# Performance work log

Hardware: AMD Instinct MI355X
Metric: run time of the kernel (lower is better)

## Reference

```python
import jax, jax.numpy as jnp
import numpy as np

HEADS = 16
DIM = 1024


def setup_inputs() -> dict:
    key = jax.random.key(0)
    ks = jax.random.split(key, 9)
    B, N, D = 2, 2048, DIM
    s = 1.0 / np.sqrt(D)
    x = jax.random.normal(ks[0], (B, N, D), dtype=jnp.float32)
    Wq = jax.random.normal(ks[1], (D, D), dtype=jnp.float32) * s
    Wk = jax.random.normal(ks[2], (D, D), dtype=jnp.float32) * s
    Wv = jax.random.normal(ks[3], (D, D), dtype=jnp.float32) * s
    Wo = jax.random.normal(ks[4], (D, D), dtype=jnp.float32) * s
    bq = jax.random.normal(ks[5], (D,), dtype=jnp.float32) * 0.01
    bk = jax.random.normal(ks[6], (D,), dtype=jnp.float32) * 0.01
    bv = jax.random.normal(ks[7], (D,), dtype=jnp.float32) * 0.01
    bo = jax.random.normal(ks[8], (D,), dtype=jnp.float32) * 0.01
    return {"x": x, "Wq": Wq, "bq": bq, "Wk": Wk, "bk": bk,
            "Wv": Wv, "bv": bv, "Wo": Wo, "bo": bo}


def reference(x, Wq, bq, Wk, bk, Wv, bv, Wo, bo):
    B, N, D = x.shape
    H = HEADS
    hd = D // H
    scale = hd ** (-0.5)
    # projections; split heads -> [B, H, N, hd]
    q = (x @ Wq + bq).reshape(B, N, H, hd).transpose(0, 2, 1, 3)
    k = (x @ Wk + bk).reshape(B, N, H, hd).transpose(0, 2, 1, 3)
    v = (x @ Wv + bv).reshape(B, N, H, hd).transpose(0, 2, 1, 3)
    # full [B, H, N, N] scores (faithful to naive torch implementation)
    attn = jnp.einsum('bhqd,bhkd->bhqk', q, k) * scale
    attn = jax.nn.softmax(attn, axis=-1)
    # dropout is identity in eval mode
    out = jnp.einsum('bhqk,bhkd->bhqd', attn, v)
    out = out.transpose(0, 2, 1, 3).reshape(B, N, D)
    return out @ Wo + bo
```

## Files before the change

### kernel.cpp

```cpp
#include <hip/hip_runtime.h>

#define HEADS 16
#define HD 64
#define SEQ 2048
#define DMODEL 1024
#define BATCH 2
#define MTOT (BATCH*SEQ)
#define KVB 64
#define NKH 16

typedef unsigned short u16;
typedef __bf16 bf16;
typedef bf16 bf16x8 __attribute__((ext_vector_type(8)));
typedef float f32x4 __attribute__((ext_vector_type(4)));
typedef float f32x16 __attribute__((ext_vector_type(16)));
typedef unsigned short u16x8 __attribute__((ext_vector_type(8)));
typedef unsigned short u16x4 __attribute__((ext_vector_type(4)));

static __device__ __forceinline__ u16 f2bf(float f) {
  bf16 b = (bf16)f;
  return __builtin_bit_cast(u16, b);
}

static __device__ __forceinline__ void async16(u16* lds_base, const u16* g) {
  __builtin_amdgcn_global_load_lds(
      (const __attribute__((address_space(1))) unsigned int*)g,
      (__attribute__((address_space(3))) unsigned int*)lds_base,
      16, 0, 0);
}

__global__ __launch_bounds__(256) void k_cvt(const float* __restrict__ in,
                                             u16* __restrict__ out, int n8) {
  int i = blockIdx.x * blockDim.x + threadIdx.x;
  if (i >= n8) return;
  const float4* p = (const float4*)(in + (size_t)i * 8);
  float4 a = p[0], b = p[1];
  u16x8 r;
  r[0] = f2bf(a.x); r[1] = f2bf(a.y); r[2] = f2bf(a.z); r[3] = f2bf(a.w);
  r[4] = f2bf(b.x); r[5] = f2bf(b.y); r[6] = f2bf(b.z); r[7] = f2bf(b.w);
  *(u16x8*)(out + (size_t)i * 8) = r;
}

__global__ __launch_bounds__(256) void k_cvtT(const float* __restrict__ W0, const float* __restrict__ W1,
                                              const float* __restrict__ W2, const float* __restrict__ W3,
                                              u16* __restrict__ T0, u16* __restrict__ T1,
                                              u16* __restrict__ T2, u16* __restrict__ T3) {
  const float* W = blockIdx.z == 0 ? W0 : blockIdx.z == 1 ? W1 : blockIdx.z == 2 ? W2 : W3;
  u16*         T = blockIdx.z == 0 ? T0 : blockIdx.z == 1 ? T1 : blockIdx.z == 2 ? T2 : T3;
  __shared__ u16 tile[64 * 68];
  int t = threadIdx.x;
  int kb = blockIdx.y * 64, nb = blockIdx.x * 64;
#pragma unroll
  for (int i = 0; i < 4; ++i) {
    int c = t * 4 + i;
    int row = c >> 4;
    int c4 = c & 15;
    float4 v = *(const float4*)&W[(size_t)(kb + row) * DMODEL + nb + c4 * 4];
    tile[row * 68 + c4 * 4 + 0] = f2bf(v.x);
    tile[row * 68 + c4 * 4 + 1] = f2bf(v.y);
    tile[row * 68 + c4 * 4 + 2] = f2bf(v.z);
    tile[row * 68 + c4 * 4 + 3] = f2bf(v.w);
  }
  __syncthreads();
#pragma unroll
  for (int i = 0; i < 2; ++i) {
    int c = t * 2 + i;
    int n = c >> 3;
    int k8 = c & 7;
    u16x8 v;
#pragma unroll
    for (int e = 0; e < 8; ++e) v[e] = tile[(k8 * 8 + e) * 68 + n];
    *(u16x8*)&T[(size_t)(nb + n) * DMODEL + kb + k8 * 8] = v;
  }
}

template <int MODE>
__global__ __launch_bounds__(256) void k_gemm(
    const u16* __restrict__ A,
    const u16* __restrict__ BT0, const u16* __restrict__ BT1, const u16* __restrict__ BT2,
    const float* __restrict__ b0, const float* __restrict__ b1, const float* __restrict__ b2,
    void* __restrict__ O0, void* __restrict__ O1, void* __restrict__ O2,
    int M, int N, int K) {
  const u16* BT = blockIdx.z == 0 ? BT0 : blockIdx.z == 1 ? BT1 : BT2;
  const float* bias = blockIdx.z == 0 ? b0 : blockIdx.z == 1 ? b1 : b2;
  void* Out = blockIdx.z == 0 ? O0 : blockIdx.z == 1 ? O1 : O2;

  __shared__ u16 Ads[2][128 * 32];
  __shared__ u16 Bds[2][128 * 32];
  int tid = threadIdx.x, wid = tid >> 6, lane = tid & 63;
  int r = lane & 15, g = lane >> 4;
  int wm = wid >> 1, wn = wid & 1;
  int m0 = blockIdx.y * 128, n0 = blockIdx.x * 128;

  f32x4 acc[4][4];
  f32x4 zero4 = {0.f, 0.f, 0.f, 0.f};
#pragma unroll
  for (int mt = 0; mt < 4; ++mt)
#pragma unroll
    for (int nt = 0; nt < 4; ++nt) acc[mt][nt] = zero4;

  int srow = lane >> 2;
  int scb = lane & 3;

  auto STAGE = [&](int b, int k0) {
#pragma unroll
    for (int tt = 0; tt < 2; ++tt) {
      int inst = wid * 2 + tt;
      int row = inst * 16 + srow;
      async16(&Ads[b][inst * 512], &A[(size_t)(m0 + row) * K + k0 + scb * 8]);
      async16(&Bds[b][inst * 512], &BT[(size_t)(n0 + row) * K + k0 + scb * 8]);
    }
  };

  auto BODY = [&](int buf, int k0) {
    if (k0 + 32 < K) STAGE(buf ^ 1, k0 + 32);
    bf16x8 af[4], bfv[4];
#pragma unroll
    for (int mt = 0; mt < 4; ++mt)
      af[mt] = *(const bf16x8*)&Ads[buf][(wm * 64 + mt * 16 + r) * 32 + g * 8];
#pragma unroll
    for (int nt = 0; nt < 4; ++nt)
      bfv[nt] = *(const bf16x8*)&Bds[buf][(wn * 64 + nt * 16 + r) * 32 + g * 8];
#pragma unroll
    for (int mt = 0; mt < 4; ++mt)
#pragma unroll
      for (int nt = 0; nt < 4; ++nt)
        acc[mt][nt] = __builtin_amdgcn_mfma_f32_16x16x32_bf16(af[mt], bfv[nt], acc[mt][nt], 0, 0, 0);
    asm volatile("s_waitcnt vmcnt(0)" ::: "memory");
    __builtin_amdgcn_sched_barrier(0);
    __builtin_amdgcn_s_barrier();
    __builtin_amdgcn_sched_barrier(0);
  };

  STAGE(0, 0);
  asm volatile("s_waitcnt vmcnt(0)" ::: "memory");
  __builtin_amdgcn_sched_barrier(0);
  __builtin_amdgcn_s_barrier();
  __builtin_amdgcn_sched_barrier(0);

  for (int k0 = 0; k0 < K; k0 += 64) {
    BODY(0, k0);
    BODY(1, k0 + 32);
  }

  const float qs = 0.18033688011112042f;
#pragma unroll
  for (int nt = 0; nt < 4; ++nt) {
    int col = n0 + wn * 64 + nt * 16 + r;
    float bv = bias[col];
#pragma unroll
    for (int mt = 0; mt < 4; ++mt) {
      int rowb = m0 + wm * 64 + mt * 16 + g * 4;
      if (MODE == 0) {
        int b = rowb >> 11;
        int h = col >> 6, d = col & (HD - 1);
        if (blockIdx.z == 2) {
          int n = rowb & (SEQ - 1);
          int np = (n & ~12) | ((n & 4) << 1) | ((n & 8) >> 1);
          u16x4 pk;
#pragma unroll
          for (int j = 0; j < 4; ++j) pk[j] = f2bf(acc[mt][nt][j] + bv);
          *(u16x4*)&((u16*)Out)[((size_t)((b * HEADS + h) * HD + d)) * SEQ + np] = pk;
        } else {
          float sc = (blockIdx.z == 0) ? qs : 1.0f;
#pragma unroll
          for (int j = 0; j < 4; ++j) {
            int row = rowb + j;
            int n = row & (SEQ - 1);
            ((u16*)Out)[((size_t)(b * HEADS + h) * SEQ + n) * HD + d] = f2bf((acc[mt][nt][j] + bv) * sc);
          }
        }
      } else {
#pragma unroll
        for (int j = 0; j < 4; ++j)
          ((float*)Out)[(size_t)(rowb + j) * N + col] = acc[mt][nt][j] + bv;
      }
    }
  }
}

__global__ __launch_bounds__(256, 2) void k_attn(const u16* __restrict__ Q,
                                                 const u16* __restrict__ Kg,
                                                 const u16* __restrict__ Vt,
                                                 u16* __restrict__ Oa) {
  __shared__ u16 lds[2][2][2][KVB * 64];

  int tid = threadIdx.x, wid = tid >> 6, lane = tid & 63;
  int l31 = lane & 31, hi = lane >> 5;
  int h = wid >> 1, s = wid & 1;

  int fid = blockIdx.y * gridDim.x + blockIdx.x;
  int swz = (fid & 7) * 64 + (fid >> 3);
  int qt = swz & 15;
  int bh = swz >> 4;

  const size_t kbase = (size_t)bh * SEQ * HD;
  const size_t vbase = (size_t)bh * HD * SEQ;
  int qA = qt * 128 + s * 64;

  bf16x8 qfA[4], qfB[4];
#pragma unroll
  for (int db = 0; db < 4; ++db) {
    qfA[db] = *(const bf16x8*)&Q[kbase + (size_t)(qA + l31) * HD + db * 16 + hi * 8];
    qfB[db] = *(const bf16x8*)&Q[kbase + (size_t)(qA + 32 + l31) * HD + db * 16 + hi * 8];
  }

  int swz7 = l31 & 7;
  int coff[4];
#pragma unroll
  for (int i = 0; i < 4; ++i) coff[i] = ((2 * i + hi) ^ swz7) * 8;

  f32x16 zero16 = {0.f,0.f,0.f,0.f,0.f,0.f,0.f,0.f,0.f,0.f,0.f,0.f,0.f,0.f,0.f,0.f};
  f32x16 oa0A = zero16, oa1A = zero16, lA = zero16;
  f32x16 oa0B = zero16, oa1B = zero16, lB = zero16;

  u16x8 onesb;
#pragma unroll
  for (int e = 0; e < 8; ++e) onesb[e] = 0x3F80;
  bf16x8 ones = __builtin_bit_cast(bf16x8, onesb);

  auto STAGE = [&](int b, int kc) {
    int kof = (h * NKH + kc) * KVB;
#pragma unroll
    for (int i = 0; i < 4; ++i) {
      int inst = s * 4 + i;
      int rr = inst * 8 + (lane >> 3);
      int ch = (lane & 7) ^ (rr & 7);
      async16(&lds[b][h][0][inst * 512], &Kg[kbase + (size_t)(kof + rr) * HD + ch * 8]);
      async16(&lds[b][h][1][inst * 512], &Vt[vbase + (size_t)rr * SEQ + kof + ch * 8]);
    }
  };

  auto BODY = [&](int buf, int kc) {
    if (kc + 1 < NKH) STAGE(buf ^ 1, kc + 1);

    const u16* Kb = &lds[buf][h][0][0];
    const u16* Vb = &lds[buf][h][1][0];

    f32x16 s0A = zero16, s1A = zero16, s0B = zero16, s1B = zero16;
#pragma unroll
    for (int db = 0; db < 4; ++db) {
      bf16x8 kf0 = *(const bf16x8*)&Kb[l31 * 64 + coff[db]];
      bf16x8 kf1 = *(const bf16x8*)&Kb[2048 + l31 * 64 + coff[db]];
      s0A = __builtin_amdgcn_mfma_f32_32x32x16_bf16(kf0, qfA[db], s0A, 0, 0, 0);
      s1A = __builtin_amdgcn_mfma_f32_32x32x16_bf16(kf1, qfA[db], s1A, 0, 0, 0);
      s0B = __builtin_amdgcn_mfma_f32_32x32x16_bf16(kf0, qfB[db], s0B, 0, 0, 0);
      s1B = __builtin_amdgcn_mfma_f32_32x32x16_bf16(kf1, qfB[db], s1B, 0, 0, 0);
    }

#pragma unroll
    for (int t = 0; t < 4; ++t) {
      u16x8 pkA, pkB;
#pragma unroll
      for (int e = 0; e < 8; ++e) {
        float svA = (t & 2) ? ((t & 1) ? s1A[8 + e] : s1A[e])
                            : ((t & 1) ? s0A[8 + e] : s0A[e]);
        float svB = (t & 2) ? ((t & 1) ? s1B[8 + e] : s1B[e])
                            : ((t & 1) ? s0B[8 + e] : s0B[e]);
        pkA[e] = f2bf(__builtin_amdgcn_exp2f(svA));
        pkB[e] = f2bf(__builtin_amdgcn_exp2f(svB));
      }
      bf16x8 paA = __builtin_bit_cast(bf16x8, pkA);
      bf16x8 paB = __builtin_bit_cast(bf16x8, pkB);

      bf16x8 vf0 = *(const bf16x8*)&Vb[l31 * 64 + coff[t]];
      bf16x8 vf1 = *(const bf16x8*)&Vb[2048 + l31 * 64 + coff[t]];
      lA   = __builtin_amdgcn_mfma_f32_32x32x16_bf16(paA, ones, lA, 0, 0, 0);
      oa0A = __builtin_amdgcn_mfma_f32_32x32x16_bf16(paA, vf0, oa0A, 0, 0, 0);
      oa1A = __builtin_amdgcn_mfma_f32_32x32x16_bf16(paA, vf1, oa1A, 0, 0, 0);
      lB   = __builtin_amdgcn_mfma_f32_32x32x16_bf16(paB, ones, lB, 0, 0, 0);
      oa0B = __builtin_amdgcn_mfma_f32_32x32x16_bf16(paB, vf0, oa0B, 0, 0, 0);
      oa1B = __builtin_amdgcn_mfma_f32_32x32x16_bf16(paB, vf1, oa1B, 0, 0, 0);
    }

    asm volatile("s_waitcnt vmcnt(0)" ::: "memory");
    __builtin_amdgcn_sched_barrier(0);
    __builtin_amdgcn_s_barrier();
    __builtin_amdgcn_sched_barrier(0);
  };

  STAGE(0, 0);
  asm volatile("s_waitcnt vmcnt(0)" ::: "memory");
  __builtin_amdgcn_sched_barrier(0);
  __builtin_amdgcn_s_barrier();
  __builtin_amdgcn_sched_barrier(0);

  for (int kc = 0; kc < NKH; kc += 2) {
    BODY(0, kc);
    BODY(1, kc + 1);
  }

  float* cf = (float*)&lds[0][0][0][0];
  int b = bh >> 4, hh = bh & 15;

  if (h == 1) {
#pragma unroll
    for (int r = 0; r < 16; ++r) {
      cf[s * 3072 + r * 64 + lane]        = oa0A[r];
      cf[s * 3072 + 1024 + r * 64 + lane] = oa1A[r];
      cf[s * 3072 + 2048 + r * 64 + lane] = lA[r];
    }
  }
  __syncthreads();
  if (h == 0) {
#pragma unroll
    for (int reg = 0; reg < 16; ++reg) {
      float o0 = oa0A[reg] + cf[s * 3072 + reg * 64 + lane];
      float o1 = oa1A[reg] + cf[s * 3072 + 1024 + reg * 64 + lane];
      float lv = lA[reg]   + cf[s * 3072 + 2048 + reg * 64 + lane];
      float inv = 1.0f / lv;
      int q = qA + (reg & 3) + 8 * (reg >> 2) + 4 * hi;
      size_t rowoff = ((size_t)(b * SEQ + q)) * DMODEL + hh * HD;
      Oa[rowoff + l31]      = f2bf(o0 * inv);
      Oa[rowoff + 32 + l31] = f2bf(o1 * inv);
    }
  }
  __syncthreads();
  if (h == 1) {
#pragma unroll
    for (int r = 0; r < 16; ++r) {
      cf[s * 3072 + r * 64 + lane]        = oa0B[r];
      cf[s * 3072 + 1024 + r * 64 + lane] = oa1B[r];
      cf[s * 3072 + 2048 + r * 64 + lane] = lB[r];
    }
  }
  __syncthreads();
  if (h == 0) {
#pragma unroll
    for (int reg = 0; reg < 16; ++reg) {
      float o0 = oa0B[reg] + cf[s * 3072 + reg * 64 + lane];
      float o1 = oa1B[reg] + cf[s * 3072 + 1024 + reg * 64 + lane];
      float lv = lB[reg]   + cf[s * 3072 + 2048 + reg * 64 + lane];
      float inv = 1.0f / lv;
      int q = qA + 32 + (reg & 3) + 8 * (reg >> 2) + 4 * hi;
      size_t rowoff = ((size_t)(b * SEQ + q)) * DMODEL + hh * HD;
      Oa[rowoff + l31]      = f2bf(o0 * inv);
      Oa[rowoff + 32 + l31] = f2bf(o1 * inv);
    }
  }
}

extern "C" void kernel_launch(void* const* d_in, const int* in_sizes, int n_in,
                              void* d_out, int out_size, void* d_ws, size_t ws_size,
                              hipStream_t stream) {
  const float* x  = (const float*)d_in[0];
  const float* Wq = (const float*)d_in[1];
  const float* bq = (const float*)d_in[2];
  const float* Wk = (const float*)d_in[3];
  const float* bk = (const float*)d_in[4];
  const float* Wv = (const float*)d_in[5];
  const float* bv = (const float*)d_in[6];
  const float* Wo = (const float*)d_in[7];
  const float* bo = (const float*)d_in[8];

  char* ws = (char*)d_ws;
  const size_t MB = 1024 * 1024;
  u16* xb    = (u16*)(ws);
  u16* wqT   = (u16*)(ws + 8 * MB);
  u16* wkT   = (u16*)(ws + 10 * MB);
  u16* wvT   = (u16*)(ws + 12 * MB);
  u16* woT   = (u16*)(ws + 14 * MB);
  u16* qbuf  = (u16*)(ws + 16 * MB);
  u16* kbuf  = (u16*)(ws + 24 * MB);
  u16* vbufT = (u16*)(ws + 32 * MB);
  u16* abuf  = (u16*)(ws + 40 * MB);

  k_cvt<<<2048, 256, 0, stream>>>(x, xb, (MTOT * DMODEL) / 8);
  k_cvtT<<<dim3(16, 16, 4), 256, 0, stream>>>(Wq, Wk, Wv, Wo, wqT, wkT, wvT, woT);
  k_gemm<0><<<dim3(DMODEL / 128, MTOT / 128, 3), 256, 0, stream>>>(
      xb, wqT, wkT, wvT, bq, bk, bv, qbuf, kbuf, vbufT, MTOT, DMODEL, DMODEL);
  k_attn<<<dim3(SEQ / 128, BATCH * HEADS), 256, 0, stream>>>(qbuf, kbuf, vbufT, abuf);
  k_gemm<1><<<dim3(DMODEL / 128, MTOT / 128, 1), 256, 0, stream>>>(
      abuf, woT, woT, woT, bo, bo, bo, d_out, d_out, d_out, MTOT, DMODEL, DMODEL);
}
```

Measured before the change: 114.1 us.

## Load K/V fragments directly from global memory instead of LDS double-buffering

```diff
diff --git a/kernel.cpp b/kernel.cpp
--- a/kernel.cpp
+++ b/kernel.cpp
@@ -183,7 +183,7 @@
                                                  const u16* __restrict__ Kg,
                                                  const u16* __restrict__ Vt,
                                                  u16* __restrict__ Oa) {
-  __shared__ u16 lds[2][2][2][KVB * 64];
+  __shared__ float cf[2 * 3072];
 
   int tid = threadIdx.x, wid = tid >> 6, lane = tid & 63;
   int l31 = lane & 31, hi = lane >> 5;
@@ -205,11 +205,6 @@
     qfB[db] = *(const bf16x8*)&Q[kbase + (size_t)(qA + 32 + l31) * HD + db * 16 + hi * 8];
   }
 
-  int swz7 = l31 & 7;
-  int coff[4];
-#pragma unroll
-  for (int i = 0; i < 4; ++i) coff[i] = ((2 * i + hi) ^ swz7) * 8;
-
   f32x16 zero16 = {0.f,0.f,0.f,0.f,0.f,0.f,0.f,0.f,0.f,0.f,0.f,0.f,0.f,0.f,0.f,0.f};
   f32x16 oa0A = zero16, oa1A = zero16, lA = zero16;
   f32x16 oa0B = zero16, oa1B = zero16, lB = zero16;
@@ -219,33 +214,25 @@
   for (int e = 0; e < 8; ++e) onesb[e] = 0x3F80;
   bf16x8 ones = __builtin_bit_cast(bf16x8, onesb);
 
-  auto STAGE = [&](int b, int kc) {
+  for (int kc = 0; kc < NKH; ++kc) {
     int kof = (h * NKH + kc) * KVB;
-#pragma unroll
-    for (int i = 0; i < 4; ++i) {
-      int inst = s * 4 + i;
-      int rr = inst * 8 + (lane >> 3);
-      int ch = (lane & 7) ^ (rr & 7);
-      async16(&lds[b][h][0][inst * 512], &Kg[kbase + (size_t)(kof + rr) * HD + ch * 8]);
-      async16(&lds[b][h][1][inst * 512], &Vt[vbase + (size_t)rr * SEQ + kof + ch * 8]);
-    }
-  };
-
-  auto BODY = [&](int buf, int kc) {
-    if (kc + 1 < NKH) STAGE(buf ^ 1, kc + 1);
-
-    const u16* Kb = &lds[buf][h][0][0];
-    const u16* Vb = &lds[buf][h][1][0];
+    const u16* Kt = Kg + kbase + (size_t)kof * HD;
+    const u16* Vp = Vt + vbase + kof;
+
+    bf16x8 kf0[4], kf1[4];
+#pragma unroll
+    for (int db = 0; db < 4; ++db) {
+      kf0[db] = *(const bf16x8*)&Kt[(size_t)l31 * HD + (2 * db + hi) * 8];
+      kf1[db] = *(const bf16x8*)&Kt[(size_t)(32 + l31) * HD + (2 * db + hi) * 8];
+    }
 
     f32x16 s0A = zero16, s1A = zero16, s0B = zero16, s1B = zero16;
 #pragma unroll
     for (int db = 0; db < 4; ++db) {
-      bf16x8 kf0 = *(const bf16x8*)&Kb[l31 * 64 + coff[db]];
-      bf16x8 kf1 = *(const bf16x8*)&Kb[2048 + l31 * 64 + coff[db]];
-      s0A = __builtin_amdgcn_mfma_f32_32x32x16_bf16(kf0, qfA[db], s0A, 0, 0, 0);
-      s1A = __builtin_amdgcn_mfma_f32_32x32x16_bf16(kf1, qfA[db], s1A, 0, 0, 0);
-      s0B = __builtin_amdgcn_mfma_f32_32x32x16_bf16(kf0, qfB[db], s0B, 0, 0, 0);
-      s1B = __builtin_amdgcn_mfma_f32_32x32x16_bf16(kf1, qfB[db], s1B, 0, 0, 0);
+      s0A = __builtin_amdgcn_mfma_f32_32x32x16_bf16(kf0[db], qfA[db], s0A, 0, 0, 0);
+      s1A = __builtin_amdgcn_mfma_f32_32x32x16_bf16(kf1[db], qfA[db], s1A, 0, 0, 0);
+      s0B = __builtin_amdgcn_mfma_f32_32x32x16_bf16(kf0[db], qfB[db], s0B, 0, 0, 0);
+      s1B = __builtin_amdgcn_mfma_f32_32x32x16_bf16(kf1[db], qfB[db], s1B, 0, 0, 0);
     }
 
 #pragma unroll
@@ -263,8 +250,8 @@
       bf16x8 paA = __builtin_bit_cast(bf16x8, pkA);
       bf16x8 paB = __builtin_bit_cast(bf16x8, pkB);
 
-      bf16x8 vf0 = *(const bf16x8*)&Vb[l31 * 64 + coff[t]];
-      bf16x8 vf1 = *(const bf16x8*)&Vb[2048 + l31 * 64 + coff[t]];
+      bf16x8 vf0 = *(const bf16x8*)&Vp[(size_t)l31 * SEQ + (2 * t + hi) * 8];
+      bf16x8 vf1 = *(const bf16x8*)&Vp[(size_t)(32 + l31) * SEQ + (2 * t + hi) * 8];
       lA   = __builtin_amdgcn_mfma_f32_32x32x16_bf16(paA, ones, lA, 0, 0, 0);
       oa0A = __builtin_amdgcn_mfma_f32_32x32x16_bf16(paA, vf0, oa0A, 0, 0, 0);
       oa1A = __builtin_amdgcn_mfma_f32_32x32x16_bf16(paA, vf1, oa1A, 0, 0, 0);
@@ -272,25 +259,8 @@
       oa0B = __builtin_amdgcn_mfma_f32_32x32x16_bf16(paB, vf0, oa0B, 0, 0, 0);
       oa1B = __builtin_amdgcn_mfma_f32_32x32x16_bf16(paB, vf1, oa1B, 0, 0, 0);
     }
-
-    asm volatile("s_waitcnt vmcnt(0)" ::: "memory");
-    __builtin_amdgcn_sched_barrier(0);
-    __builtin_amdgcn_s_barrier();
-    __builtin_amdgcn_sched_barrier(0);
-  };
-
-  STAGE(0, 0);
-  asm volatile("s_waitcnt vmcnt(0)" ::: "memory");
-  __builtin_amdgcn_sched_barrier(0);
-  __builtin_amdgcn_s_barrier();
-  __builtin_amdgcn_sched_barrier(0);
-
-  for (int kc = 0; kc < NKH; kc += 2) {
-    BODY(0, kc);
-    BODY(1, kc + 1);
-  }
-
-  float* cf = (float*)&lds[0][0][0][0];
+  }
+
   int b = bh >> 4, hh = bh & 15;
 
   if (h == 1) {
```

New measurement: 136.9 us. 20.1% more time.
